# Kernel tuning notes

Hardware: AMD Instinct MI355X
Metric: run time of the kernel (lower is better)

## Reference

```python
import jax, jax.numpy as jnp
import numpy as np

N_NODES = 100000
FEAT_DIM = 3
HID = 128
S1 = 50  # enc1 neighbor samples
S2 = 10  # enc2 neighbor samples


def setup_inputs() -> dict:
    key = jax.random.key(0)
    ks = jax.random.split(key, 12)
    inp = {
        "nodes": jnp.arange(N_NODES, dtype=jnp.int64) if jax.config.jax_enable_x64 else jnp.arange(N_NODES, dtype=jnp.int32),
        "features": jax.random.normal(ks[0], (N_NODES, FEAT_DIM), dtype=jnp.float32),
        "neigh1": jax.random.randint(ks[1], (N_NODES, S1), 0, N_NODES),
        "neigh2": jax.random.randint(ks[2], (N_NODES, S2), 0, N_NODES),
        "W1": jax.random.normal(ks[3], (HID, FEAT_DIM), dtype=jnp.float32) * 0.5,
        "W2": jax.random.normal(ks[4], (HID, HID), dtype=jnp.float32) * 0.08,
        "w_a": jax.random.normal(ks[5], (128, HID + 1), dtype=jnp.float32) * 0.08,
        "b_a": jax.random.normal(ks[6], (128,), dtype=jnp.float32) * 0.01,
        "w_b": jax.random.normal(ks[7], (64, 128), dtype=jnp.float32) * 0.08,
        "b_b": jax.random.normal(ks[8], (64,), dtype=jnp.float32) * 0.01,
        "w_c": jax.random.normal(ks[9], (1, 64), dtype=jnp.float32) * 0.1,
        "b_c": jax.random.normal(ks[10], (1,), dtype=jnp.float32) * 0.01,
        "partition_size": 500,
        "n_partition_edges": 137,
    }
    return inp


def reference(nodes, features, neigh1, neigh2, W1, W2, w_a, b_a, w_b, b_b, w_c, b_c,
              partition_size, n_partition_edges):
    # ---- enc1 (GraphSAGE mean, gcn=True: self node included in mean) over all nodes
    nf1 = features[neigh1]                       # [N, S1, F] irregular gather
    agg1 = (nf1.sum(axis=1) + features) / (neigh1.shape[1] + 1)  # [N, F]
    h1 = jax.nn.relu(agg1 @ W1.T)                # [N, HID]

    # ---- enc2 over the query nodes
    nf2 = h1[neigh2[nodes]]                      # [n, S2, HID] irregular gather
    agg2 = (nf2.sum(axis=1) + h1[nodes]) / (neigh2.shape[1] + 1)  # [n, HID]
    emb = jax.nn.relu(agg2 @ W2.T)               # [n, HID]

    # ---- append remaining-space column, MLP, softmax over all nodes (dim 0)
    remaining_space = jnp.asarray(partition_size - n_partition_edges, dtype=emb.dtype)
    col = jnp.full((emb.shape[0], 1), remaining_space, dtype=emb.dtype)
    x = jnp.concatenate([emb, col], axis=1)      # [n, HID+1]
    x = jax.nn.relu(x @ w_a.T + b_a)
    x = jax.nn.relu(x @ w_b.T + b_b)
    scores = (x @ w_c.T + b_c)[:, 0]             # [n]
    return jax.nn.softmax(scores, axis=0)
```

## Files before the change

kernel.cpp:

```cpp
#include <hip/hip_runtime.h>
#include <math.h>

#define N_NODES 100000
#define S1 50
#define S2 10
#define HID 128
#define NT 32
#define AST 34

#define W2_ELEMS   (128 * 128)
#define WA_ELEMS   (129 * 128)
#define WB_ELEMS   (128 * 64)
#define PAD_ELEMS  (W2_ELEMS + WA_ELEMS + WB_ELEMS)

__global__ __launch_bounds__(256) void prep_kernel(
    const float* __restrict__ feat, const int* __restrict__ neigh1,
    const float* __restrict__ W2, const float* __restrict__ w_a,
    const float* __restrict__ w_b,
    double* __restrict__ agg1d, double* __restrict__ wt)
{
    if (blockIdx.x >= 25000) {
        int i = (blockIdx.x - 25000) * 256 + threadIdx.x;
        if (i < W2_ELEMS) {
            int k = i >> 7, o = i & 127;
            wt[i] = (double)W2[o * 128 + k];
        } else if (i < W2_ELEMS + WA_ELEMS) {
            int j = i - W2_ELEMS;
            int k = j >> 7, o = j & 127;
            wt[i] = (double)w_a[o * 129 + k];
        } else if (i < PAD_ELEMS) {
            int j = i - W2_ELEMS - WA_ELEMS;
            int k = j >> 6, o = j & 63;
            wt[i] = (double)w_b[o * 128 + k];
        }
        return;
    }
    const int wid  = threadIdx.x >> 6;
    const int lane = threadIdx.x & 63;
    const int n = blockIdx.x * 4 + wid;
    if (n >= N_NODES) return;

    double f0 = 0.0, f1 = 0.0, f2 = 0.0;
    if (lane < S1) {
        int j = neigh1[n * S1 + lane];
        f0 = (double)feat[j * 3 + 0];
        f1 = (double)feat[j * 3 + 1];
        f2 = (double)feat[j * 3 + 2];
    } else if (lane == S1) {
        f0 = (double)feat[n * 3 + 0];
        f1 = (double)feat[n * 3 + 1];
        f2 = (double)feat[n * 3 + 2];
    }
    #pragma unroll
    for (int off = 32; off > 0; off >>= 1) {
        f0 += __shfl_down(f0, off);
        f1 += __shfl_down(f1, off);
        f2 += __shfl_down(f2, off);
    }
    if (lane == 0) {
        const double r51 = 1.0 / 51.0;
        agg1d[n * 3 + 0] = f0 * r51;
        agg1d[n * 3 + 1] = f1 * r51;
        agg1d[n * 3 + 2] = f2 * r51;
    }
}

__global__ __launch_bounds__(128, 1) void enc2_mlp_kernel(
    const int* __restrict__ nodes, const int* __restrict__ neigh2,
    const double* __restrict__ agg1d,
    const float* __restrict__ W1, const double* __restrict__ wt,
    const float* __restrict__ b_a, const float* __restrict__ b_b,
    const float* __restrict__ w_c, const float* __restrict__ b_c,
    const int* __restrict__ psz, const int* __restrict__ npe,
    double* __restrict__ scoresd)
{
    __shared__ __align__(16) double sX[HID * AST];
    double* sG = sX;

    const double* __restrict__ Wt2 = wt;
    const double* __restrict__ Wta = wt + W2_ELEMS;
    const double* __restrict__ Wtb = wt + W2_ELEMS + WA_ELEMS;

    const int tid  = threadIdx.x;
    const int base = blockIdx.x * NT;

    for (int t = tid; t < NT * (S2 + 1); t += 128) {
        int ns = t / 11, j = t - ns * 11;
        int node = nodes[base + ns];
        int src  = (j == 0) ? node : neigh2[node * S2 + (j - 1)];
        sG[t * 4 + 0] = agg1d[src * 3 + 0];
        sG[t * 4 + 1] = agg1d[src * 3 + 1];
        sG[t * 4 + 2] = agg1d[src * 3 + 2];
    }
    __syncthreads();

    {
        const int n = tid & 31;
        double g0[11], g1[11], g2[11];
        #pragma unroll
        for (int j = 0; j < 11; j++) {
            g0[j] = sG[(n * 11 + j) * 4 + 0];
            g1[j] = sG[(n * 11 + j) * 4 + 1];
            g2[j] = sG[(n * 11 + j) * 4 + 2];
        }
        __syncthreads();
        const int part = tid >> 5;
        #pragma unroll
        for (int s = 0; s < 32; s++) {
            int t = part * 32 + s;
            double wx = (double)W1[t * 3 + 0];
            double wy = (double)W1[t * 3 + 1];
            double wz = (double)W1[t * 3 + 2];
            double acc = 0.0;
            #pragma unroll
            for (int j = 0; j < 11; j++)
                acc += fmax(wx * g0[j] + wy * g1[j] + wz * g2[j], 0.0);
            sX[t * AST + n] = acc / 11.0;
        }
    }
    __syncthreads();

    const int og = tid & 31;
    const int ng = tid >> 5;
    const int n0 = 8 * ng;
    const int o0 = 2 * og;

    {
        double acc[4][8] = {};
        const double* __restrict__ wk = &Wt2[o0];
        const double* __restrict__ ak = &sX[n0];
        double2 wc0 = *(const double2*)&wk[0];
        double2 wc1 = *(const double2*)&wk[64];
        double2 wd0 = *(const double2*)&wk[128];
        double2 wd1 = *(const double2*)&wk[128 + 64];
        double2 ac[4];
        #pragma unroll
        for (int i = 0; i < 4; i++) ac[i] = *(const double2*)&ak[2 * i];
        #pragma unroll 4
        for (int k = 0; k < 128; k++) {
            const int k1 = (k + 1) & 127;
            const int k2 = (k + 2) & 127;
            double2 wn0 = *(const double2*)&wk[k2 * 128];
            double2 wn1 = *(const double2*)&wk[k2 * 128 + 64];
            double2 an[4];
            #pragma unroll
            for (int i = 0; i < 4; i++)
                an[i] = *(const double2*)&ak[k1 * AST + 2 * i];
            #pragma unroll
            for (int i = 0; i < 4; i++) {
                acc[0][2*i]   += wc0.x * ac[i].x; acc[0][2*i+1] += wc0.x * ac[i].y;
                acc[1][2*i]   += wc0.y * ac[i].x; acc[1][2*i+1] += wc0.y * ac[i].y;
                acc[2][2*i]   += wc1.x * ac[i].x; acc[2][2*i+1] += wc1.x * ac[i].y;
                acc[3][2*i]   += wc1.y * ac[i].x; acc[3][2*i+1] += wc1.y * ac[i].y;
            }
            wc0 = wd0; wc1 = wd1; wd0 = wn0; wd1 = wn1;
            #pragma unroll
            for (int i = 0; i < 4; i++) ac[i] = an[i];
        }
        __syncthreads();
        #pragma unroll
        for (int i = 0; i < 4; i++) {
            int o = (i < 2) ? (o0 + i) : (64 + o0 + i - 2);
            #pragma unroll
            for (int j = 0; j < 4; j++) {
                double2 v = { fmax(acc[i][2*j], 0.0), fmax(acc[i][2*j+1], 0.0) };
                *(double2*)&sX[o * AST + n0 + 2 * j] = v;
            }
        }
    }
    __syncthreads();

    {
        double acc[4][8] = {};
        const double* __restrict__ wk = &Wta[o0];
        const double* __restrict__ ak = &sX[n0];
        double2 wc0 = *(const double2*)&wk[0];
        double2 wc1 = *(const double2*)&wk[64];
        double2 wd0 = *(const double2*)&wk[128];
        double2 wd1 = *(const double2*)&wk[128 + 64];
        double2 ac[4];
        #pragma unroll
        for (int i = 0; i < 4; i++) ac[i] = *(const double2*)&ak[2 * i];
        #pragma unroll 4
        for (int k = 0; k < 128; k++) {
            const int k1 = (k + 1) & 127;
            const int k2 = (k + 2) & 127;
            double2 wn0 = *(const double2*)&wk[k2 * 128];
            double2 wn1 = *(const double2*)&wk[k2 * 128 + 64];
            double2 an[4];
            #pragma unroll
            for (int i = 0; i < 4; i++)
                an[i] = *(const double2*)&ak[k1 * AST + 2 * i];
            #pragma unroll
            for (int i = 0; i < 4; i++) {
                acc[0][2*i]   += wc0.x * ac[i].x; acc[0][2*i+1] += wc0.x * ac[i].y;
                acc[1][2*i]   += wc0.y * ac[i].x; acc[1][2*i+1] += wc0.y * ac[i].y;
                acc[2][2*i]   += wc1.x * ac[i].x; acc[2][2*i+1] += wc1.x * ac[i].y;
                acc[3][2*i]   += wc1.y * ac[i].x; acc[3][2*i+1] += wc1.y * ac[i].y;
            }
            wc0 = wd0; wc1 = wd1; wd0 = wn0; wd1 = wn1;
            #pragma unroll
            for (int i = 0; i < 4; i++) ac[i] = an[i];
        }
        const double rem = (double)(psz[0] - npe[0]);
        double2 rl = *(const double2*)&Wta[128 * 128 + o0];
        double2 rh = *(const double2*)&Wta[128 * 128 + 64 + o0];
        const double ad[4] = {
            rl.x * rem + (double)b_a[o0],
            rl.y * rem + (double)b_a[o0 + 1],
            rh.x * rem + (double)b_a[64 + o0],
            rh.y * rem + (double)b_a[64 + o0 + 1] };
        __syncthreads();
        #pragma unroll
        for (int i = 0; i < 4; i++) {
            int o = (i < 2) ? (o0 + i) : (64 + o0 + i - 2);
            #pragma unroll
            for (int j = 0; j < 4; j++) {
                double2 v = { fmax(acc[i][2*j] + ad[i], 0.0),
                              fmax(acc[i][2*j+1] + ad[i], 0.0) };
                *(double2*)&sX[o * AST + n0 + 2 * j] = v;
            }
        }
    }
    __syncthreads();

    {
        double acc[2][8] = {};
        const double* __restrict__ wk = &Wtb[o0];
        const double* __restrict__ ak = &sX[n0];
        double2 wc = *(const double2*)&wk[0];
        double2 wd = *(const double2*)&wk[64];
        double2 ac[4];
        #pragma unroll
        for (int i = 0; i < 4; i++) ac[i] = *(const double2*)&ak[2 * i];
        #pragma unroll 4
        for (int k = 0; k < 128; k++) {
            const int k1 = (k + 1) & 127;
            const int k2 = (k + 2) & 127;
            double2 wn = *(const double2*)&wk[k2 * 64];
            double2 an[4];
            #pragma unroll
            for (int i = 0; i < 4; i++)
                an[i] = *(const double2*)&ak[k1 * AST + 2 * i];
            #pragma unroll
            for (int i = 0; i < 4; i++) {
                acc[0][2*i]   += wc.x * ac[i].x; acc[0][2*i+1] += wc.x * ac[i].y;
                acc[1][2*i]   += wc.y * ac[i].x; acc[1][2*i+1] += wc.y * ac[i].y;
            }
            wc = wd; wd = wn;
            #pragma unroll
            for (int i = 0; i < 4; i++) ac[i] = an[i];
        }
        __syncthreads();
        #pragma unroll
        for (int i = 0; i < 2; i++) {
            int o = o0 + i;
            double bb = (double)b_b[o];
            #pragma unroll
            for (int j = 0; j < 4; j++) {
                double2 v = { fmax(acc[i][2*j] + bb, 0.0),
                              fmax(acc[i][2*j+1] + bb, 0.0) };
                *(double2*)&sX[o * AST + n0 + 2 * j] = v;
            }
        }
    }
    __syncthreads();

    {
        const int j4 = tid & 3, ns = tid >> 2;
        double v = 0.0;
        #pragma unroll
        for (int r = 0; r < 16; r++)
            v += (double)w_c[j4 + 4 * r] * sX[(j4 + 4 * r) * AST + ns];
        v += __shfl_down(v, 2);
        v += __shfl_down(v, 1);
        if (j4 == 0)
            scoresd[base + ns] = v + (double)b_c[0];
    }
}

__global__ __launch_bounds__(256) void reduce_max_kernel(
    const double* __restrict__ s, double* __restrict__ pmax)
{
    __shared__ double red[4];
    const int tid = threadIdx.x;
    double m = -INFINITY;
    for (int i = blockIdx.x * 256 + tid; i < N_NODES; i += gridDim.x * 256)
        m = fmax(m, s[i]);
    #pragma unroll
    for (int off = 32; off > 0; off >>= 1) m = fmax(m, __shfl_down(m, off));
    if ((tid & 63) == 0) red[tid >> 6] = m;
    __syncthreads();
    if (tid == 0)
        pmax[blockIdx.x] = fmax(fmax(red[0], red[1]), fmax(red[2], red[3]));
}

__global__ __launch_bounds__(256) void exp_sum_kernel(
    double* __restrict__ s, const double* __restrict__ pmax,
    double* __restrict__ psum)
{
    __shared__ double red[4];
    const int tid = threadIdx.x;
    double m = pmax[tid];
    #pragma unroll
    for (int off = 32; off > 0; off >>= 1) m = fmax(m, __shfl_down(m, off));
    if ((tid & 63) == 0) red[tid >> 6] = m;
    __syncthreads();
    m = fmax(fmax(red[0], red[1]), fmax(red[2], red[3]));
    __syncthreads();

    double acc = 0.0;
    for (int i = blockIdx.x * 256 + tid; i < N_NODES; i += gridDim.x * 256) {
        double e = exp(s[i] - m);
        s[i] = e;
        acc += e;
    }
    #pragma unroll
    for (int off = 32; off > 0; off >>= 1) acc += __shfl_down(acc, off);
    if ((tid & 63) == 0) red[tid >> 6] = acc;
    __syncthreads();
    if (tid == 0)
        psum[blockIdx.x] = (red[0] + red[1]) + (red[2] + red[3]);
}

__global__ __launch_bounds__(256) void scale_kernel(
    const double* __restrict__ e, const double* __restrict__ psum,
    float* __restrict__ out)
{
    __shared__ double red[4];
    const int tid = threadIdx.x;
    double acc = psum[tid];
    #pragma unroll
    for (int off = 32; off > 0; off >>= 1) acc += __shfl_down(acc, off);
    if ((tid & 63) == 0) red[tid >> 6] = acc;
    __syncthreads();
    const double invS = 1.0 / ((red[0] + red[1]) + (red[2] + red[3]));
    const int i = blockIdx.x * 256 + tid;
    if (i < N_NODES) out[i] = (float)(e[i] * invS);
}

extern "C" void kernel_launch(void* const* d_in, const int* in_sizes, int n_in,
                              void* d_out, int out_size, void* d_ws, size_t ws_size,
                              hipStream_t stream)
{
    const int*   nodes = (const int*)  d_in[0];
    const float* feat  = (const float*)d_in[1];
    const int*   n1    = (const int*)  d_in[2];
    const int*   n2    = (const int*)  d_in[3];
    const float* W1    = (const float*)d_in[4];
    const float* W2    = (const float*)d_in[5];
    const float* w_a   = (const float*)d_in[6];
    const float* b_a   = (const float*)d_in[7];
    const float* w_b   = (const float*)d_in[8];
    const float* b_b   = (const float*)d_in[9];
    const float* w_c   = (const float*)d_in[10];
    const float* b_c   = (const float*)d_in[11];
    const int*   psz   = (const int*)  d_in[12];
    const int*   npe   = (const int*)  d_in[13];
    float* out = (float*)d_out;

    double* agg1d   = (double*)d_ws;
    double* scoresd = agg1d + (size_t)N_NODES * 3;
    double* pmax    = scoresd + N_NODES;
    double* psum    = pmax + 256;
    double* wt      = psum + 256;

    const int pad_blocks = (PAD_ELEMS + 255) / 256;
    prep_kernel<<<25000 + pad_blocks, 256, 0, stream>>>(
        feat, n1, W2, w_a, w_b, agg1d, wt);
    enc2_mlp_kernel<<<N_NODES / NT, 128, 0, stream>>>(
        nodes, n2, agg1d, W1, wt, b_a, b_b, w_c, b_c, psz, npe, scoresd);
    reduce_max_kernel<<<256, 256, 0, stream>>>(scoresd, pmax);
    exp_sum_kernel<<<256, 256, 0, stream>>>(scoresd, pmax, psum);
    scale_kernel<<<(N_NODES + 255) / 256, 256, 0, stream>>>(scoresd, psum, out);
}
```

Measured before the change: 371.6 us.

## Pack features to float4, fuse softmax max into MLP via atomics

```diff
diff --git a/kernel.cpp b/kernel.cpp
--- a/kernel.cpp
+++ b/kernel.cpp
@@ -13,44 +13,56 @@
 #define WB_ELEMS   (128 * 64)
 #define PAD_ELEMS  (W2_ELEMS + WA_ELEMS + WB_ELEMS)
 
-__global__ __launch_bounds__(256) void prep_kernel(
-    const float* __restrict__ feat, const int* __restrict__ neigh1,
+__device__ __forceinline__ unsigned long long dkey(double d) {
+    unsigned long long u = __double_as_longlong(d);
+    return (u & 0x8000000000000000ULL) ? ~u : (u | 0x8000000000000000ULL);
+}
+__device__ __forceinline__ double dunkey(unsigned long long k) {
+    return (k & 0x8000000000000000ULL)
+        ? __longlong_as_double(k & 0x7FFFFFFFFFFFFFFFULL)
+        : __longlong_as_double(~k);
+}
+
+__global__ __launch_bounds__(256) void pack_kernel(
+    const float* __restrict__ feat,
     const float* __restrict__ W2, const float* __restrict__ w_a,
     const float* __restrict__ w_b,
-    double* __restrict__ agg1d, double* __restrict__ wt)
-{
-    if (blockIdx.x >= 25000) {
-        int i = (blockIdx.x - 25000) * 256 + threadIdx.x;
-        if (i < W2_ELEMS) {
-            int k = i >> 7, o = i & 127;
-            wt[i] = (double)W2[o * 128 + k];
-        } else if (i < W2_ELEMS + WA_ELEMS) {
-            int j = i - W2_ELEMS;
-            int k = j >> 7, o = j & 127;
-            wt[i] = (double)w_a[o * 129 + k];
-        } else if (i < PAD_ELEMS) {
-            int j = i - W2_ELEMS - WA_ELEMS;
-            int k = j >> 6, o = j & 63;
-            wt[i] = (double)w_b[o * 128 + k];
-        }
-        return;
-    }
+    double* __restrict__ wt, float4* __restrict__ feat4,
+    unsigned long long* __restrict__ gmaxu, double* __restrict__ gsum)
+{
+    int i = blockIdx.x * 256 + threadIdx.x;
+    if (i == 0) { gmaxu[0] = 0ULL; gsum[0] = 0.0; }
+    if (i < W2_ELEMS) {
+        int k = i >> 7, o = i & 127;
+        wt[i] = (double)W2[o * 128 + k];
+    } else if (i < W2_ELEMS + WA_ELEMS) {
+        int j = i - W2_ELEMS;
+        int k = j >> 7, o = j & 127;
+        wt[i] = (double)w_a[o * 129 + k];
+    } else if (i < PAD_ELEMS) {
+        int j = i - W2_ELEMS - WA_ELEMS;
+        int k = j >> 6, o = j & 63;
+        wt[i] = (double)w_b[o * 128 + k];
+    } else if (i < PAD_ELEMS + N_NODES) {
+        int n = i - PAD_ELEMS;
+        float4 v = { feat[n * 3 + 0], feat[n * 3 + 1], feat[n * 3 + 2], 0.0f };
+        feat4[n] = v;
+    }
+}
+
+__global__ __launch_bounds__(256) void gather_kernel(
+    const float4* __restrict__ feat4, const int* __restrict__ neigh1,
+    double* __restrict__ agg1d)
+{
     const int wid  = threadIdx.x >> 6;
     const int lane = threadIdx.x & 63;
     const int n = blockIdx.x * 4 + wid;
     if (n >= N_NODES) return;
 
-    double f0 = 0.0, f1 = 0.0, f2 = 0.0;
-    if (lane < S1) {
-        int j = neigh1[n * S1 + lane];
-        f0 = (double)feat[j * 3 + 0];
-        f1 = (double)feat[j * 3 + 1];
-        f2 = (double)feat[j * 3 + 2];
-    } else if (lane == S1) {
-        f0 = (double)feat[n * 3 + 0];
-        f1 = (double)feat[n * 3 + 1];
-        f2 = (double)feat[n * 3 + 2];
-    }
+    float4 v = { 0.f, 0.f, 0.f, 0.f };
+    if (lane < S1)       v = feat4[neigh1[n * S1 + lane]];
+    else if (lane == S1) v = feat4[n];
+    double f0 = (double)v.x, f1 = (double)v.y, f2 = (double)v.z;
     #pragma unroll
     for (int off = 32; off > 0; off >>= 1) {
         f0 += __shfl_down(f0, off);
@@ -72,9 +84,10 @@
     const float* __restrict__ b_a, const float* __restrict__ b_b,
     const float* __restrict__ w_c, const float* __restrict__ b_c,
     const int* __restrict__ psz, const int* __restrict__ npe,
-    double* __restrict__ scoresd)
+    double* __restrict__ scoresd, unsigned long long* __restrict__ gmaxu)
 {
     __shared__ __align__(16) double sX[HID * AST];
+    __shared__ double sS[2];
     double* sG = sX;
 
     const double* __restrict__ Wt2 = wt;
@@ -274,40 +287,27 @@
             v += (double)w_c[j4 + 4 * r] * sX[(j4 + 4 * r) * AST + ns];
         v += __shfl_down(v, 2);
         v += __shfl_down(v, 1);
+        double sc = v + (double)b_c[0];
         if (j4 == 0)
-            scoresd[base + ns] = v + (double)b_c[0];
-    }
-}
-
-__global__ __launch_bounds__(256) void reduce_max_kernel(
-    const double* __restrict__ s, double* __restrict__ pmax)
+            scoresd[base + ns] = sc;
+        double vh = (j4 == 0) ? sc : -HUGE_VAL;
+        #pragma unroll
+        for (int off = 32; off > 0; off >>= 1)
+            vh = fmax(vh, __shfl_down(vh, off));
+        if ((tid & 63) == 0) sS[tid >> 6] = vh;
+        __syncthreads();
+        if (tid == 0)
+            atomicMax(gmaxu, dkey(fmax(sS[0], sS[1])));
+    }
+}
+
+__global__ __launch_bounds__(256) void exp_sum_kernel(
+    double* __restrict__ s, const unsigned long long* __restrict__ gmaxu,
+    double* __restrict__ gsum)
 {
     __shared__ double red[4];
     const int tid = threadIdx.x;
-    double m = -INFINITY;
-    for (int i = blockIdx.x * 256 + tid; i < N_NODES; i += gridDim.x * 256)
-        m = fmax(m, s[i]);
-    #pragma unroll
-    for (int off = 32; off > 0; off >>= 1) m = fmax(m, __shfl_down(m, off));
-    if ((tid & 63) == 0) red[tid >> 6] = m;
-    __syncthreads();
-    if (tid == 0)
-        pmax[blockIdx.x] = fmax(fmax(red[0], red[1]), fmax(red[2], red[3]));
-}
-
-__global__ __launch_bounds__(256) void exp_sum_kernel(
-    double* __restrict__ s, const double* __restrict__ pmax,
-    double* __restrict__ psum)
-{
-    __shared__ double red[4];
-    const int tid = threadIdx.x;
-    double m = pmax[tid];
-    #pragma unroll
-    for (int off = 32; off > 0; off >>= 1) m = fmax(m, __shfl_down(m, off));
-    if ((tid & 63) == 0) red[tid >> 6] = m;
-    __syncthreads();
-    m = fmax(fmax(red[0], red[1]), fmax(red[2], red[3]));
-    __syncthreads();
+    const double m = dunkey(gmaxu[0]);
 
     double acc = 0.0;
     for (int i = blockIdx.x * 256 + tid; i < N_NODES; i += gridDim.x * 256) {
@@ -320,23 +320,19 @@
     if ((tid & 63) == 0) red[tid >> 6] = acc;
     __syncthreads();
     if (tid == 0)
-        psum[blockIdx.x] = (red[0] + red[1]) + (red[2] + red[3]);
+        atomicAdd(gsum, (red[0] + red[1]) + (red[2] + red[3]));
 }
 
 __global__ __launch_bounds__(256) void scale_kernel(
-    const double* __restrict__ e, const double* __restrict__ psum,
+    const double* __restrict__ e, const double* __restrict__ gsum,
     float* __restrict__ out)
 {
-    __shared__ double red[4];
+    __shared__ double sv;
     const int tid = threadIdx.x;
-    double acc = psum[tid];
-    #pragma unroll
-    for (int off = 32; off > 0; off >>= 1) acc += __shfl_down(acc, off);
-    if ((tid & 63) == 0) red[tid >> 6] = acc;
-    __syncthreads();
-    const double invS = 1.0 / ((red[0] + red[1]) + (red[2] + red[3]));
+    if (tid == 0) sv = 1.0 / gsum[0];
+    __syncthreads();
     const int i = blockIdx.x * 256 + tid;
-    if (i < N_NODES) out[i] = (float)(e[i] * invS);
+    if (i < N_NODES) out[i] = (float)(e[i] * sv);
 }
 
 extern "C" void kernel_launch(void* const* d_in, const int* in_sizes, int n_in,
@@ -361,16 +357,18 @@
 
     double* agg1d   = (double*)d_ws;
     double* scoresd = agg1d + (size_t)N_NODES * 3;
-    double* pmax    = scoresd + N_NODES;
-    double* psum    = pmax + 256;
-    double* wt      = psum + 256;
-
-    const int pad_blocks = (PAD_ELEMS + 255) / 256;
-    prep_kernel<<<25000 + pad_blocks, 256, 0, stream>>>(
-        feat, n1, W2, w_a, w_b, agg1d, wt);
+    unsigned long long* gmaxu =
+        (unsigned long long*)(scoresd + N_NODES);
+    double* gsum    = (double*)(gmaxu + 1);
+    double* wt      = scoresd + N_NODES + 16;
+    float4* feat4   = (float4*)(wt + PAD_ELEMS);
+
+    const int pack_blocks = (PAD_ELEMS + N_NODES + 255) / 256;
+    pack_kernel<<<pack_blocks, 256, 0, stream>>>(
+        feat, W2, w_a, w_b, wt, feat4, gmaxu, gsum);
+    gather_kernel<<<25000, 256, 0, stream>>>(feat4, n1, agg1d);
     enc2_mlp_kernel<<<N_NODES / NT, 128, 0, stream>>>(
-        nodes, n2, agg1d, W1, wt, b_a, b_b, w_c, b_c, psz, npe, scoresd);
-    reduce_max_kernel<<<256, 256, 0, stream>>>(scoresd, pmax);
-    exp_sum_kernel<<<256, 256, 0, stream>>>(scoresd, pmax, psum);
-    scale_kernel<<<(N_NODES + 255) / 256, 256, 0, stream>>>(scoresd, psum, out);
-}
+        nodes, n2, agg1d, W1, wt, b_a, b_b, w_c, b_c, psz, npe, scoresd, gmaxu);
+    exp_sum_kernel<<<256, 256, 0, stream>>>(scoresd, gmaxu, gsum);
+    scale_kernel<<<(N_NODES + 255) / 256, 256, 0, stream>>>(scoresd, gsum, out);
+}
```

Result: no change. 371.9 us (+0.1%).
